# Performance work log

Measured on AMD Instinct MI355X. Metric: run time of the kernel, lower is better.

Reference implementation:

```python
import jax, jax.numpy as jnp
import numpy as np

N_EMBD = 1024
N_HEAD = 16
HEAD_SIZE = N_EMBD // N_HEAD  # 64
BLOCK_SIZE = 2048
HIDDEN = 2 * N_EMBD  # SwiGLU hidden
LN_EPS = 1e-5


def layernorm(x, w, b):
    m = jnp.mean(x, axis=-1, keepdims=True)
    v = jnp.mean(jnp.square(x - m), axis=-1, keepdims=True)
    return (x - m) * jax.lax.rsqrt(v + LN_EPS) * w + b


def rotate_half(x):
    # interleaved halves, exactly as the torch code: stack((-x2, x1)).reshape
    x1 = x[..., 0::2]
    x2 = x[..., 1::2]
    return jnp.stack((-x2, x1), axis=-1).reshape(x.shape)


def rope_tables(T, hd):
    inv_freq = 1.0 / (10000.0 ** (jnp.arange(0, hd, 2, dtype=jnp.float32) / hd))
    t = jnp.arange(T, dtype=jnp.float32)
    freqs = t[:, None] * inv_freq[None, :]           # [T, hd/2]
    emb = jnp.concatenate([freqs, freqs], axis=-1)   # [T, hd]
    return jnp.cos(emb), jnp.sin(emb)


def setup_inputs() -> dict:
    key = jax.random.key(0)
    ks = jax.random.split(key, 12)
    s = 0.02
    d = {
        "x": jax.random.normal(ks[0], (2, BLOCK_SIZE, N_EMBD), dtype=jnp.float32),
        "ln1_w": jnp.ones((N_EMBD,), jnp.float32),
        "ln1_b": jnp.zeros((N_EMBD,), jnp.float32),
        "ln2_w": jnp.ones((N_EMBD,), jnp.float32),
        "ln2_b": jnp.zeros((N_EMBD,), jnp.float32),
        # per-head projections, stored (H, C, hd); equivalent to x @ W.T in torch
        "Wq": jax.random.normal(ks[1], (N_HEAD, N_EMBD, HEAD_SIZE), jnp.float32) * s,
        "Wk": jax.random.normal(ks[2], (N_HEAD, N_EMBD, HEAD_SIZE), jnp.float32) * s,
        "Wv": jax.random.normal(ks[3], (N_HEAD, N_EMBD, HEAD_SIZE), jnp.float32) * s,
        "proj_w": jax.random.normal(ks[4], (N_EMBD, N_EMBD), jnp.float32) * s,
        "proj_b": jnp.zeros((N_EMBD,), jnp.float32),
        # SwiGLU MLP
        "w_w": jax.random.normal(ks[5], (N_EMBD, HIDDEN), jnp.float32) * s,
        "w_b": jnp.zeros((HIDDEN,), jnp.float32),
        "v_w": jax.random.normal(ks[6], (N_EMBD, HIDDEN), jnp.float32) * s,
        "v_b": jnp.zeros((HIDDEN,), jnp.float32),
        "p_w": jax.random.normal(ks[7], (HIDDEN, N_EMBD), jnp.float32) * s,
        "p_b": jnp.zeros((N_EMBD,), jnp.float32),
    }
    return d


def reference(x, ln1_w, ln1_b, ln2_w, ln2_b, Wq, Wk, Wv, proj_w, proj_b,
              w_w, w_b, v_w, v_b, p_w, p_b):
    B, T, C = x.shape
    # --- attention sub-block ---
    h = layernorm(x, ln1_w, ln1_b)
    q = jnp.einsum('btc,hcd->bhtd', h, Wq)
    k = jnp.einsum('btc,hcd->bhtd', h, Wk)
    v = jnp.einsum('btc,hcd->bhtd', h, Wv)
    cos, sin = rope_tables(T, HEAD_SIZE)  # [T, hd]
    cos = cos[None, None]
    sin = sin[None, None]
    q = q * cos + rotate_half(q) * sin
    k = k * cos + rotate_half(k) * sin
    scale = 1.0 / jnp.sqrt(jnp.float32(HEAD_SIZE))
    scores = jnp.einsum('bhtd,bhsd->bhts', q, k) * scale  # [B,H,T,T]
    causal = jnp.tril(jnp.ones((T, T), dtype=bool))
    scores = jnp.where(causal[None, None], scores, -jnp.inf)
    att = jax.nn.softmax(scores, axis=-1)
    o = jnp.einsum('bhts,bhsd->bhtd', att, v)
    o = o.transpose(0, 2, 1, 3).reshape(B, T, C)  # concat heads
    sa = o @ proj_w + proj_b
    x = x + sa
    # --- SwiGLU FFN sub-block ---
    h2 = layernorm(x, ln2_w, ln2_b)
    a = h2 @ w_w + w_b
    a = a * jax.nn.sigmoid(a)  # swish
    b = h2 @ v_w + v_b
    ff = (a * b) @ p_w + p_b
    return x + ff
```

## Files before the change

### kernel.cpp

```cpp
#include <hip/hip_runtime.h>
#include <math.h>

#define N_EMBD    1024
#define N_HEAD    16
#define HEAD_SIZE 64
#define T_SEQ     2048
#define BATCH     2
#define HIDDEN    2048
#define ROWS      4096

typedef __attribute__((ext_vector_type(8))) short bf16x8;
typedef __attribute__((ext_vector_type(4))) float f32x4;
typedef __attribute__((ext_vector_type(16))) float f32x16;
typedef unsigned short u16;

__device__ __forceinline__ u16 f2bf(float x) {
    union { float f; unsigned u; } v; v.f = x;
    unsigned r = v.u + 0x7fffu + ((v.u >> 16) & 1u);
    return (u16)(r >> 16);
}
__device__ __forceinline__ float bf2f(u16 h) {
    union { unsigned u; float f; } v; v.u = ((unsigned)h) << 16;
    return v.f;
}
__device__ __forceinline__ unsigned cvtpk_bf16(float lo, float hi) {
    unsigned r;
    asm volatile("v_cvt_pk_bf16_f32 %0, %1, %2" : "=v"(r) : "v"(lo), "v"(hi));
    return r;
}
__device__ __forceinline__ void gload16(const void* g, void* lds) {
    __builtin_amdgcn_global_load_lds((const __attribute__((address_space(1))) void*)g,
                                     (__attribute__((address_space(3))) void*)lds, 16, 0, 0);
}

__device__ __forceinline__ void wtrans_body(const float* s, u16* d, int ldS, int ldD,
                                            int k0, int n0, float Ts[64][65])
{
    const int tid = threadIdx.x;
    const int rr = tid >> 4, c4 = (tid & 15) * 4;
#pragma unroll
    for (int i = 0; i < 4; i++) {
        float4 v = *(const float4*)(s + (size_t)(k0 + rr + i * 16) * ldS + n0 + c4);
        Ts[rr + i * 16][c4 + 0] = v.x;
        Ts[rr + i * 16][c4 + 1] = v.y;
        Ts[rr + i * 16][c4 + 2] = v.z;
        Ts[rr + i * 16][c4 + 3] = v.w;
    }
    __syncthreads();
    const int nr = tid >> 2, kc = (tid & 3) * 16;
#pragma unroll
    for (int j = 0; j < 4; j++) {
        u16 t0 = f2bf(Ts[kc + j * 4 + 0][nr]);
        u16 t1 = f2bf(Ts[kc + j * 4 + 1][nr]);
        u16 t2 = f2bf(Ts[kc + j * 4 + 2][nr]);
        u16 t3 = f2bf(Ts[kc + j * 4 + 3][nr]);
        *(ushort4*)(d + (size_t)(n0 + nr) * ldD + k0 + kc + j * 4) = make_ushort4(t0, t1, t2, t3);
    }
}

__global__ __launch_bounds__(256) void wtrans_all(const float* __restrict__ Wq, const float* __restrict__ Wk,
                                                  const float* __restrict__ Wv, const float* __restrict__ ww,
                                                  const float* __restrict__ vv, const float* __restrict__ pw,
                                                  const float* __restrict__ ppw,
                                                  u16* __restrict__ Wqkv, u16* __restrict__ wwT,
                                                  u16* __restrict__ vvT, u16* __restrict__ pwT,
                                                  u16* __restrict__ ppT)
{
    __shared__ float Ts[64][65];
    const int b = blockIdx.x;
    const float* s; u16* d; int ldS, ldD, k0, n0;
    if (b < 768) {
        const int z = b >> 4;
        k0 = (b & 15) * 64; n0 = 0;
        const int which = z >> 4;
        s = (which == 0 ? Wq : which == 1 ? Wk : Wv) + (size_t)(z & 15) * 65536;
        d = Wqkv + (size_t)z * 65536;
        ldS = 64; ldD = 1024;
    } else if (b < 1792) {
        const int b2 = b - 768, z = b2 >> 4;
        k0 = (b2 & 15) * 64; n0 = (z & 31) * 64;
        s = (z >> 5) ? vv : ww; d = (z >> 5) ? vvT : wwT;
        ldS = 2048; ldD = 1024;
    } else if (b < 2048) {
        const int b3 = b - 1792;
        k0 = (b3 & 15) * 64; n0 = (b3 >> 4) * 64;
        s = pw; d = pwT; ldS = 1024; ldD = 1024;
    } else {
        const int b4 = b - 2048;
        k0 = (b4 & 31) * 64; n0 = (b4 >> 5) * 64;
        s = ppw; d = ppT; ldS = 1024; ldD = 2048;
    }
    wtrans_body(s, d, ldS, ldD, k0, n0, Ts);
}

__global__ __launch_bounds__(256) void ln_kernel(const float* __restrict__ x,
                                                 const float* __restrict__ w,
                                                 const float* __restrict__ b,
                                                 u16* __restrict__ out)
{
    const int row = blockIdx.x;
    const int tid = threadIdx.x;
    const float* xr = x + (size_t)row * N_EMBD;
    float4 v = *(const float4*)(xr + tid * 4);
    float s  = v.x + v.y + v.z + v.w;
    float s2 = v.x*v.x + v.y*v.y + v.z*v.z + v.w*v.w;
#pragma unroll
    for (int off = 32; off; off >>= 1) {
        s  += __shfl_xor(s, off);
        s2 += __shfl_xor(s2, off);
    }
    __shared__ float ss[4], ss2[4];
    if ((tid & 63) == 0) { ss[tid >> 6] = s; ss2[tid >> 6] = s2; }
    __syncthreads();
    s  = ss[0] + ss[1] + ss[2] + ss[3];
    s2 = ss2[0] + ss2[1] + ss2[2] + ss2[3];
    const float mean = s * (1.0f / N_EMBD);
    const float var  = s2 * (1.0f / N_EMBD) - mean * mean;
    const float rstd = rsqrtf(var + 1e-5f);
    float4 wv = *(const float4*)(w + tid * 4);
    float4 bv = *(const float4*)(b + tid * 4);
    ushort4 st = make_ushort4(f2bf((v.x - mean) * rstd * wv.x + bv.x),
                              f2bf((v.y - mean) * rstd * wv.y + bv.y),
                              f2bf((v.z - mean) * rstd * wv.z + bv.z),
                              f2bf((v.w - mean) * rstd * wv.w + bv.w));
    *(ushort4*)(out + (size_t)row * N_EMBD + tid * 4) = st;
}

__global__ __launch_bounds__(256) void rope_kernel(u16* __restrict__ q, u16* __restrict__ k)
{
    const int u = blockIdx.x * 256 + threadIdx.x;
    const int i  = u & 31;
    const int t  = (u >> 5) & (T_SEQ - 1);
    const int bh = u >> 16;
    const size_t base = ((size_t)bh * T_SEQ + t) * HEAD_SIZE + 2 * i;
    const float L = 0.28782313662425572f;
    const float QS = 0.125f * 1.44269504088896f;
    const int i0 = (2 * i) & 31, i1 = (2 * i + 1) & 31;
    float c0, s0, c1, s1;
    sincosf((float)t * __expf(-(float)i0 * L), &s0, &c0);
    sincosf((float)t * __expf(-(float)i1 * L), &s1, &c1);
    float a0 = bf2f(q[base]), a1 = bf2f(q[base + 1]);
    q[base]     = f2bf((a0 * c0 - a1 * s0) * QS);
    q[base + 1] = f2bf((a1 * c1 + a0 * s1) * QS);
    float b0 = bf2f(k[base]), b1 = bf2f(k[base + 1]);
    k[base]     = f2bf(b0 * c0 - b1 * s0);
    k[base + 1] = f2bf(b1 * c1 + b0 * s1);
}

__global__ __launch_bounds__(256) void gemm_br(const u16* __restrict__ A, const u16* __restrict__ Bt,
                                               const float* __restrict__ bias, const float* __restrict__ resid,
                                               float* __restrict__ Cf,
                                               int N, int K)
{
    __shared__ __align__(16) u16 As[2][128 * 64];
    __shared__ __align__(16) u16 Bs[2][64 * 64];
    const int tid = threadIdx.x, w = tid >> 6, l = tid & 63, l15 = l & 15, l4 = l >> 4;
    const int wm = w >> 1, wn = w & 1;
    const int n0 = blockIdx.x * 64, m0 = blockIdx.y * 128;
    f32x4 acc[4][2] = {};
    const int NT = K >> 6;

    auto stage = [&](int buf, int k0) {
#pragma unroll
        for (int c = 0; c < 4; c++) {
            const int slot = c * 256 + tid;
            const int row = slot >> 3;
            const int sw = ((slot & 7) * 16) ^ ((row & 7) << 4);
            gload16((const char*)(A + (size_t)(m0 + row) * K + k0) + sw, (char*)&As[buf][0] + slot * 16);
        }
#pragma unroll
        for (int c = 0; c < 2; c++) {
            const int slot = c * 256 + tid;
            const int row = slot >> 3;
            const int sw = ((slot & 7) * 16) ^ ((row & 7) << 4);
            gload16((const char*)(Bt + (size_t)(n0 + row) * K + k0) + sw, (char*)&Bs[buf][0] + slot * 16);
        }
    };

    stage(0, 0);
    __syncthreads();
    int cur = 0;
    for (int t = 0; t < NT; t++) {
        if (t + 1 < NT) stage(cur ^ 1, (t + 1) << 6);
#pragma unroll
        for (int ks = 0; ks < 2; ks++) {
            const int cb = ks * 64 + l4 * 16;
            bf16x8 af[4], bf[2];
#pragma unroll
            for (int mt = 0; mt < 4; mt++) {
                const int row = wm * 64 + mt * 16 + l15;
                af[mt] = *(const bf16x8*)((const char*)&As[cur][0] + row * 128 + (cb ^ ((row & 7) << 4)));
            }
#pragma unroll
            for (int u = 0; u < 2; u++) {
                const int row = wn * 32 + u * 16 + l15;
                bf[u] = *(const bf16x8*)((const char*)&Bs[cur][0] + row * 128 + (cb ^ ((row & 7) << 4)));
            }
#pragma unroll
            for (int mt = 0; mt < 4; mt++)
#pragma unroll
                for (int u = 0; u < 2; u++)
                    acc[mt][u] = __builtin_amdgcn_mfma_f32_16x16x32_bf16(af[mt], bf[u], acc[mt][u], 0, 0, 0);
        }
        __syncthreads();
        cur ^= 1;
    }
#pragma unroll
    for (int mt = 0; mt < 4; mt++) {
#pragma unroll
        for (int u = 0; u < 2; u++) {
            const int n = n0 + wn * 32 + u * 16 + l15;
            const float bi = bias[n];
#pragma unroll
            for (int r = 0; r < 4; r++) {
                const int m = m0 + wm * 64 + mt * 16 + l4 * 4 + r;
                const size_t idx = (size_t)m * N + n;
                Cf[idx] = acc[mt][u][r] + bi + resid[idx];
            }
        }
    }
}

__global__ __launch_bounds__(256, 4) void gemm_qkv(const u16* __restrict__ A, const u16* __restrict__ Bt,
                                                   u16* __restrict__ qo, u16* __restrict__ ko, u16* __restrict__ vto)
{
    __shared__ __align__(16) u16 As[2][64 * 64];
    __shared__ __align__(16) u16 Bs[2][64 * 64];
    const int tid = threadIdx.x, w = tid >> 6, l = tid & 63, l15 = l & 15, l4 = l >> 4;
    const int wm = w >> 1, wn = w & 1;
    const int n0 = blockIdx.x * 128, m0 = blockIdx.y * 128;
    const int K = N_EMBD;
    f32x4 acc[4][4] = {};
    const int NT = K >> 5;

    auto stage = [&](int buf, int k0) {
#pragma unroll
        for (int c = 0; c < 2; c++) {
            const int slot = c * 256 + tid;
            const int r2 = slot >> 3;
            const int w16u = (slot & 7) ^ (r2 & 7);
            const int grow = (w16u >> 2) * 64 + r2;
            const int kc = w16u & 3;
            gload16(A  + (size_t)(m0 + grow) * K + k0 + kc * 8, (char*)&As[buf][0] + slot * 16);
            gload16(Bt + (size_t)(n0 + grow) * K + k0 + kc * 8, (char*)&Bs[buf][0] + slot * 16);
        }
    };

    stage(0, 0);
    __syncthreads();
    int cur = 0;
    for (int t = 0; t < NT; t++) {
        if (t + 1 < NT) stage(cur ^ 1, (t + 1) << 5);
        bf16x8 af[4], bf[4];
#pragma unroll
        for (int q4 = 0; q4 < 4; q4++) {
            const int ga = wm * 64 + q4 * 16 + l15;
            const int ra = ga & 63, ha = ga >> 6;
            af[q4] = *(const bf16x8*)((const char*)&As[cur][0] + ra * 128 + (((ha << 2) | l4) ^ (ra & 7)) * 16);
            const int gb = wn * 64 + q4 * 16 + l15;
            const int rb = gb & 63, hb = gb >> 6;
            bf[q4] = *(const bf16x8*)((const char*)&Bs[cur][0] + rb * 128 + (((hb << 2) | l4) ^ (rb & 7)) * 16);
        }
#pragma unroll
        for (int mt = 0; mt < 4; mt++)
#pragma unroll
            for (int nt = 0; nt < 4; nt++)
                acc[mt][nt] = __builtin_amdgcn_mfma_f32_16x16x32_bf16(af[mt], bf[nt], acc[mt][nt], 0, 0, 0);
        __syncthreads();
        cur ^= 1;
    }
#pragma unroll
    for (int mt = 0; mt < 4; mt++) {
#pragma unroll
        for (int nt = 0; nt < 4; nt++) {
            const int n = n0 + wn * 64 + nt * 16 + l15;
            const int which = n >> 10, hd = (n >> 6) & 15, dd = n & 63;
            const int mb = m0 + wm * 64 + mt * 16 + l4 * 4;
            const int bI = mb >> 11, tq = mb & (T_SEQ - 1);
            if (which == 2) {
                ushort4 st = make_ushort4(f2bf(acc[mt][nt][0]), f2bf(acc[mt][nt][1]),
                                          f2bf(acc[mt][nt][2]), f2bf(acc[mt][nt][3]));
                *(ushort4*)(vto + ((size_t)(bI * N_HEAD + hd) * HEAD_SIZE + dd) * T_SEQ + tq) = st;
            } else {
                u16* dst = (which == 0) ? qo : ko;
#pragma unroll
                for (int r = 0; r < 4; r++)
                    dst[((size_t)(bI * N_HEAD + hd) * T_SEQ + tq + r) * HEAD_SIZE + dd] = f2bf(acc[mt][nt][r]);
            }
        }
    }
}

__global__ __launch_bounds__(256, 4) void gemm_glu(const u16* __restrict__ A, const u16* __restrict__ Bw,
                                                   const u16* __restrict__ Bv,
                                                   const float* __restrict__ wb, const float* __restrict__ vb,
                                                   u16* __restrict__ G)
{
    __shared__ __align__(16) u16 As[2][64 * 64];
    __shared__ __align__(16) u16 Bws[2][32 * 64];
    __shared__ __align__(16) u16 Bvs[2][32 * 64];
    const int tid = threadIdx.x, w = tid >> 6, l = tid & 63, l15 = l & 15, l4 = l >> 4;
    const int wm = w >> 1, wn = w & 1;
    const int n0 = blockIdx.x * 64, m0 = blockIdx.y * 128;
    const int K = N_EMBD;
    f32x4 accA[4][2] = {};
    f32x4 accB[4][2] = {};
    const int NT = K >> 5;

    auto stage = [&](int buf, int k0) {
#pragma unroll
        for (int c = 0; c < 2; c++) {
            const int slot = c * 256 + tid;
            const int r2 = slot >> 3;
            const int w16u = (slot & 7) ^ (r2 & 7);
            const int grow = (w16u >> 2) * 64 + r2;
            const int kc = w16u & 3;
            gload16(A + (size_t)(m0 + grow) * K + k0 + kc * 8, (char*)&As[buf][0] + slot * 16);
        }
        {
            const int slot = tid;
            const int r2 = slot >> 3;
            const int w16u = (slot & 7) ^ (r2 & 7);
            const int grow = (w16u >> 2) * 32 + r2;
            const int kc = w16u & 3;
            gload16(Bw + (size_t)(n0 + grow) * K + k0 + kc * 8, (char*)&Bws[buf][0] + slot * 16);
            gload16(Bv + (size_t)(n0 + grow) * K + k0 + kc * 8, (char*)&Bvs[buf][0] + slot * 16);
        }
    };

    stage(0, 0);
    __syncthreads();
    int cur = 0;
    for (int t = 0; t < NT; t++) {
        if (t + 1 < NT) stage(cur ^ 1, (t + 1) << 5);
        bf16x8 af[4], bwf[2], bvf[2];
#pragma unroll
        for (int q4 = 0; q4 < 4; q4++) {
            const int ga = wm * 64 + q4 * 16 + l15;
            const int ra = ga & 63, ha = ga >> 6;
            af[q4] = *(const bf16x8*)((const char*)&As[cur][0] + ra * 128 + (((ha << 2) | l4) ^ (ra & 7)) * 16);
        }
#pragma unroll
        for (int u = 0; u < 2; u++) {
            const int gb = wn * 32 + u * 16 + l15;
            const int rb = gb & 31, hb = gb >> 5;
            const int off = rb * 128 + (((hb << 2) | l4) ^ (rb & 7)) * 16;
            bwf[u] = *(const bf16x8*)((const char*)&Bws[cur][0] + off);
            bvf[u] = *(const bf16x8*)((const char*)&Bvs[cur][0] + off);
        }
#pragma unroll
        for (int mt = 0; mt < 4; mt++)
#pragma unroll
            for (int u = 0; u < 2; u++) {
                accA[mt][u] = __builtin_amdgcn_mfma_f32_16x16x32_bf16(af[mt], bwf[u], accA[mt][u], 0, 0, 0);
                accB[mt][u] = __builtin_amdgcn_mfma_f32_16x16x32_bf16(af[mt], bvf[u], accB[mt][u], 0, 0, 0);
            }
        __syncthreads();
        cur ^= 1;
    }
#pragma unroll
    for (int mt = 0; mt < 4; mt++) {
#pragma unroll
        for (int u = 0; u < 2; u++) {
            const int n = n0 + wn * 32 + u * 16 + l15;
            const float wbi = wb[n], vbi = vb[n];
#pragma unroll
            for (int r = 0; r < 4; r++) {
                const int m = m0 + wm * 64 + mt * 16 + l4 * 4 + r;
                const float a  = accA[mt][u][r] + wbi;
                const float bb = accB[mt][u][r] + vbi;
                G[(size_t)m * HIDDEN + n] = f2bf(a / (1.f + __expf(-a)) * bb);
            }
        }
    }
}

__global__ __launch_bounds__(256, 4) void attn_mfma(const u16* __restrict__ q, const u16* __restrict__ k,
                                                    const u16* __restrict__ vt, u16* __restrict__ o)
{
    __shared__ __align__(16) u16 Kb[2][64 * 64];
    __shared__ __align__(16) u16 Vb[2][64 * 64];
    __shared__ float ml[2][32];
    const int tid = threadIdx.x, l = tid & 63, l31 = l & 31, hh2 = (l >> 5) & 1;
    const int wid  = tid >> 6;
    const int qsub = wid >> 1;
    const int par  = wid & 1;
    const int bh  = blockIdx.x;
    const int y = blockIdx.y;
    const int qtb = ((y & 8) == 0) ? y : ((y < 16) ? 23 - y : (y < 24 ? y : 55 - y));
    const int qt  = qtb * 2 + qsub;
    const int qw0 = qt * 32;
    const int nc  = qtb + 1;
    const u16* qb  = q  + (size_t)bh * T_SEQ * HEAD_SIZE;
    const u16* kbg = k  + (size_t)bh * T_SEQ * HEAD_SIZE;
    const u16* vbg = vt + (size_t)bh * HEAD_SIZE * T_SEQ;

    bf16x8 qf[4];
    {
        const u16* qr = qb + (size_t)(qw0 + l31) * HEAD_SIZE + hh2 * 8;
#pragma unroll
        for (int kk = 0; kk < 4; kk++) qf[kk] = *(const bf16x8*)(qr + kk * 16);
    }
    bf16x8 onesf;
#pragma unroll
    for (int e = 0; e < 8; e++) onesf[e] = (short)0x3F80;

    f32x16 oacc0 = {}, oacc1 = {}, lacc = {};
    const float M0 = 20.f;

    auto stage = [&](int buf, int s0) {
#pragma unroll
        for (int c = 0; c < 2; c++) {
            const int slot = c * 256 + tid;
            const int row = slot >> 3;
            const int sw = ((slot & 7) * 16) ^ ((row & 7) << 4);
            gload16((const char*)(kbg + (size_t)(s0 + row) * HEAD_SIZE) + sw, (char*)&Kb[buf][0] + slot * 16);
        }
#pragma unroll
        for (int c = 0; c < 2; c++) {
            const int slot = c * 256 + tid;
            const int row = slot >> 3;
            const int sw = ((slot & 7) * 16) ^ ((row & 7) << 4);
            gload16((const char*)(vbg + (size_t)row * T_SEQ + s0) + sw, (char*)&Vb[buf][0] + slot * 16);
        }
    };

    stage(0, 0);
    __syncthreads();
    int cur = 0;

    for (int j = 0; j < nc; j++) {
        if (j + 1 < nc) stage(cur ^ 1, (j + 1) * 64);

        const int hc = 2 * j + par;
        if (hc <= qt) {
            f32x16 sa;
#pragma unroll
            for (int reg = 0; reg < 16; reg++) sa[reg] = -M0;
            const int row = par * 32 + l31;
            const int swz = (row & 7) << 4;
#pragma unroll
            for (int kk = 0; kk < 4; kk++) {
                const bf16x8 kf = *(const bf16x8*)((const char*)&Kb[cur][0] + row * 128 + ((kk * 32 + hh2 * 16) ^ swz));
                sa = __builtin_amdgcn_mfma_f32_32x32x16_bf16(kf, qf[kk], sa, 0, 0, 0);
            }
            if (hc == qt) {
#pragma unroll
                for (int reg = 0; reg < 16; reg++) {
                    const int R = (reg & 3) + 8 * (reg >> 2) + 4 * hh2;
                    if (R > l31) sa[reg] = -1e30f;
                }
            }
#pragma unroll
            for (int reg = 0; reg < 16; reg++) sa[reg] = exp2f(sa[reg]);

            unsigned pk[8];
#pragma unroll
            for (int jj = 0; jj < 8; jj++) pk[jj] = cvtpk_bf16(sa[2 * jj], sa[2 * jj + 1]);

#pragma unroll
            for (int st = 0; st < 2; st++) {
                const int b = st * 4;
                union { unsigned u[4]; bf16x8 v; } r;
                const unsigned s0w = (unsigned)__shfl_xor((int)pk[b + 0], 32);
                const unsigned s1w = (unsigned)__shfl_xor((int)pk[b + 1], 32);
                const unsigned s2w = (unsigned)__shfl_xor((int)pk[b + 2], 32);
                const unsigned s3w = (unsigned)__shfl_xor((int)pk[b + 3], 32);
                r.u[0] = hh2 ? s2w : pk[b + 0];
                r.u[1] = hh2 ? s3w : pk[b + 1];
                r.u[2] = hh2 ? pk[b + 2] : s0w;
                r.u[3] = hh2 ? pk[b + 3] : s1w;
                lacc = __builtin_amdgcn_mfma_f32_32x32x16_bf16(onesf, r.v, lacc, 0, 0, 0);
#pragma unroll
                for (int dt = 0; dt < 2; dt++) {
                    const int vrow = dt * 32 + l31;
                    const int vswz = (vrow & 7) << 4;
                    const int vcol = (par * 64 + st * 32 + hh2 * 16) ^ vswz;
                    const bf16x8 vf = *(const bf16x8*)((const char*)&Vb[cur][0] + vrow * 128 + vcol);
                    if (dt == 0) oacc0 = __builtin_amdgcn_mfma_f32_32x32x16_bf16(vf, r.v, oacc0, 0, 0, 0);
                    else         oacc1 = __builtin_amdgcn_mfma_f32_32x32x16_bf16(vf, r.v, oacc1, 0, 0, 0);
                }
            }
        }
        __syncthreads();
        cur ^= 1;
    }

    float* obuf = (float*)&Kb[0][0] + (size_t)qsub * 2048;
    if (par == 1) {
#pragma unroll
        for (int reg = 0; reg < 16; reg++) {
            const int R = (reg & 3) + 8 * (reg >> 2) + 4 * hh2;
            obuf[R * 32 + l31] = oacc0[reg];
            obuf[(32 + R) * 32 + l31] = oacc1[reg];
        }
        if (hh2 == 0) ml[qsub][l31] = lacc[0];
    }
    __syncthreads();
    if (par == 0) {
        const float inv = 1.f / (lacc[0] + ml[qsub][l31]);
        const int bI = bh >> 4, hd = bh & 15;
        u16* ob = o + ((size_t)(bI * T_SEQ + qw0 + l31)) * N_EMBD + hd * HEAD_SIZE;
#pragma unroll
        for (int g = 0; g < 4; g++) {
            const int d0a = g * 8 + hh2 * 4;
            float v0[4], v1[4];
#pragma unroll
            for (int r = 0; r < 4; r++) {
                const int R = d0a + r;
                v0[r] = (oacc0[4 * g + r] + obuf[R * 32 + l31]) * inv;
                v1[r] = (oacc1[4 * g + r] + obuf[(32 + R) * 32 + l31]) * inv;
            }
            *(ushort4*)(ob + d0a)      = make_ushort4(f2bf(v0[0]), f2bf(v0[1]), f2bf(v0[2]), f2bf(v0[3]));
            *(ushort4*)(ob + 32 + d0a) = make_ushort4(f2bf(v1[0]), f2bf(v1[1]), f2bf(v1[2]), f2bf(v1[3]));
        }
    }
}

extern "C" void kernel_launch(void* const* d_in, const int* in_sizes, int n_in,
                              void* d_out, int out_size, void* d_ws, size_t ws_size,
                              hipStream_t stream)
{
    (void)in_sizes; (void)n_in; (void)out_size; (void)ws_size;
    const float* x      = (const float*)d_in[0];
    const float* ln1_w  = (const float*)d_in[1];
    const float* ln1_b  = (const float*)d_in[2];
    const float* ln2_w  = (const float*)d_in[3];
    const float* ln2_b  = (const float*)d_in[4];
    const float* Wq     = (const float*)d_in[5];
    const float* Wk     = (const float*)d_in[6];
    const float* Wv     = (const float*)d_in[7];
    const float* proj_w = (const float*)d_in[8];
    const float* proj_b = (const float*)d_in[9];
    const float* w_w    = (const float*)d_in[10];
    const float* w_b    = (const float*)d_in[11];
    const float* v_w    = (const float*)d_in[12];
    const float* v_b    = (const float*)d_in[13];
    const float* p_w    = (const float*)d_in[14];
    const float* p_b    = (const float*)d_in[15];
    float* out = (float*)d_out;

    char* W = (char*)d_ws;
    u16*   Wqkv = (u16*)(W + 0);
    u16*   pwT  = (u16*)(W + 6291456);
    u16*   wwT  = (u16*)(W + 8388608);
    u16*   vvT  = (u16*)(W + 12582912);
    u16*   ppT  = (u16*)(W + 16777216);
    u16*   h    = (u16*)(W + 20971520);
    u16*   qB   = (u16*)(W + 29360128);
    u16*   kB   = (u16*)(W + 37748736);
    u16*   vtB  = (u16*)(W + 46137344);
    u16*   oB   = (u16*)(W + 54525952);
    float* x1   = (float*)(W + 62914560);
    u16*   ga   = qB;

    wtrans_all<<<2560, 256, 0, stream>>>(Wq, Wk, Wv, w_w, v_w, proj_w, p_w,
                                         Wqkv, wwT, vvT, pwT, ppT);

    ln_kernel<<<ROWS, 256, 0, stream>>>(x, ln1_w, ln1_b, h);
    gemm_qkv<<<dim3(24, 32), 256, 0, stream>>>(h, Wqkv, qB, kB, vtB);
    rope_kernel<<<(BATCH * N_HEAD * T_SEQ * 32) / 256, 256, 0, stream>>>(qB, kB);
    attn_mfma<<<dim3(BATCH * N_HEAD, T_SEQ / 64), 256, 0, stream>>>(qB, kB, vtB, oB);
    gemm_br<<<dim3(16, 32), 256, 0, stream>>>(oB, pwT, proj_b, x, x1, N_EMBD, N_EMBD);
    ln_kernel<<<ROWS, 256, 0, stream>>>(x1, ln2_w, ln2_b, h);
    gemm_glu<<<dim3(32, 32), 256, 0, stream>>>(h, wwT, vvT, w_b, v_b, ga);
    gemm_br<<<dim3(16, 32), 256, 0, stream>>>(ga, ppT, p_b, x1, out, N_EMBD, HIDDEN);
}
```

Before: 204.4 us.

## Shrink residual GEMM tiles to 64x64 and simplify attention block ordering

The bias+residual GEMM moves from 128x64 tiles with a 64-wide K step to 64x64 tiles with a 32-wide K step. Each staging load now covers both operands with a new swizzled LDS layout, launch bounds request 4 blocks per CU, and the grid doubles to 1024 blocks. This aims to fill the MI355X CUs better for the 4096x1024 outputs, at the cost of less data reuse per tile and twice as many K iterations and barriers. Attention blocks are also remapped to run the longest causal query tiles first, replacing the previous interleaved ordering.

```diff
diff --git a/kernel.cpp b/kernel.cpp
--- a/kernel.cpp
+++ b/kernel.cpp
@@ -147,73 +147,64 @@
     k[base + 1] = f2bf(b1 * c1 + b0 * s1);
 }
 
-__global__ __launch_bounds__(256) void gemm_br(const u16* __restrict__ A, const u16* __restrict__ Bt,
-                                               const float* __restrict__ bias, const float* __restrict__ resid,
-                                               float* __restrict__ Cf,
-                                               int N, int K)
-{
-    __shared__ __align__(16) u16 As[2][128 * 64];
-    __shared__ __align__(16) u16 Bs[2][64 * 64];
+__global__ __launch_bounds__(256, 4) void gemm_br(const u16* __restrict__ A, const u16* __restrict__ Bt,
+                                                  const float* __restrict__ bias, const float* __restrict__ resid,
+                                                  float* __restrict__ Cf,
+                                                  int N, int K)
+{
+    __shared__ __align__(16) u16 As[2][32 * 64];
+    __shared__ __align__(16) u16 Bs[2][32 * 64];
     const int tid = threadIdx.x, w = tid >> 6, l = tid & 63, l15 = l & 15, l4 = l >> 4;
     const int wm = w >> 1, wn = w & 1;
-    const int n0 = blockIdx.x * 64, m0 = blockIdx.y * 128;
-    f32x4 acc[4][2] = {};
-    const int NT = K >> 6;
+    const int n0 = blockIdx.x * 64, m0 = blockIdx.y * 64;
+    f32x4 acc[2][2] = {};
+    const int NT = K >> 5;
 
     auto stage = [&](int buf, int k0) {
-#pragma unroll
-        for (int c = 0; c < 4; c++) {
-            const int slot = c * 256 + tid;
-            const int row = slot >> 3;
-            const int sw = ((slot & 7) * 16) ^ ((row & 7) << 4);
-            gload16((const char*)(A + (size_t)(m0 + row) * K + k0) + sw, (char*)&As[buf][0] + slot * 16);
-        }
-#pragma unroll
-        for (int c = 0; c < 2; c++) {
-            const int slot = c * 256 + tid;
-            const int row = slot >> 3;
-            const int sw = ((slot & 7) * 16) ^ ((row & 7) << 4);
-            gload16((const char*)(Bt + (size_t)(n0 + row) * K + k0) + sw, (char*)&Bs[buf][0] + slot * 16);
-        }
+        const int slot = tid;
+        const int r2 = slot >> 3;
+        const int w16u = (slot & 7) ^ (r2 & 7);
+        const int grow = (w16u >> 2) * 32 + r2;
+        const int kc = w16u & 3;
+        gload16(A  + (size_t)(m0 + grow) * K + k0 + kc * 8, (char*)&As[buf][0] + slot * 16);
+        gload16(Bt + (size_t)(n0 + grow) * K + k0 + kc * 8, (char*)&Bs[buf][0] + slot * 16);
     };
 
     stage(0, 0);
     __syncthreads();
     int cur = 0;
     for (int t = 0; t < NT; t++) {
-        if (t + 1 < NT) stage(cur ^ 1, (t + 1) << 6);
-#pragma unroll
-        for (int ks = 0; ks < 2; ks++) {
-            const int cb = ks * 64 + l4 * 16;
-            bf16x8 af[4], bf[2];
-#pragma unroll
-            for (int mt = 0; mt < 4; mt++) {
-                const int row = wm * 64 + mt * 16 + l15;
-                af[mt] = *(const bf16x8*)((const char*)&As[cur][0] + row * 128 + (cb ^ ((row & 7) << 4)));
-            }
-#pragma unroll
-            for (int u = 0; u < 2; u++) {
-                const int row = wn * 32 + u * 16 + l15;
-                bf[u] = *(const bf16x8*)((const char*)&Bs[cur][0] + row * 128 + (cb ^ ((row & 7) << 4)));
-            }
-#pragma unroll
-            for (int mt = 0; mt < 4; mt++)
-#pragma unroll
-                for (int u = 0; u < 2; u++)
-                    acc[mt][u] = __builtin_amdgcn_mfma_f32_16x16x32_bf16(af[mt], bf[u], acc[mt][u], 0, 0, 0);
-        }
+        if (t + 1 < NT) stage(cur ^ 1, (t + 1) << 5);
+        bf16x8 af[2], bf[2];
+#pragma unroll
+        for (int mt = 0; mt < 2; mt++) {
+            const int ga = wm * 32 + mt * 16 + l15;
+            const int ra = ga & 31, ha = ga >> 5;
+            af[mt] = *(const bf16x8*)((const char*)&As[cur][0] + ra * 128 + (((ha << 2) | l4) ^ (ra & 7)) * 16);
+        }
+#pragma unroll
+        for (int u = 0; u < 2; u++) {
+            const int gb = wn * 32 + u * 16 + l15;
+            const int rb = gb & 31, hb = gb >> 5;
+            bf[u] = *(const bf16x8*)((const char*)&Bs[cur][0] + rb * 128 + (((hb << 2) | l4) ^ (rb & 7)) * 16);
+        }
+#pragma unroll
+        for (int mt = 0; mt < 2; mt++)
+#pragma unroll
+            for (int u = 0; u < 2; u++)
+                acc[mt][u] = __builtin_amdgcn_mfma_f32_16x16x32_bf16(af[mt], bf[u], acc[mt][u], 0, 0, 0);
         __syncthreads();
         cur ^= 1;
     }
 #pragma unroll
-    for (int mt = 0; mt < 4; mt++) {
+    for (int mt = 0; mt < 2; mt++) {
 #pragma unroll
         for (int u = 0; u < 2; u++) {
             const int n = n0 + wn * 32 + u * 16 + l15;
             const float bi = bias[n];
 #pragma unroll
             for (int r = 0; r < 4; r++) {
-                const int m = m0 + wm * 64 + mt * 16 + l4 * 4 + r;
+                const int m = m0 + wm * 32 + mt * 16 + l4 * 4 + r;
                 const size_t idx = (size_t)m * N + n;
                 Cf[idx] = acc[mt][u][r] + bi + resid[idx];
             }
@@ -386,8 +377,7 @@
     const int qsub = wid >> 1;
     const int par  = wid & 1;
     const int bh  = blockIdx.x;
-    const int y = blockIdx.y;
-    const int qtb = ((y & 8) == 0) ? y : ((y < 16) ? 23 - y : (y < 24 ? y : 55 - y));
+    const int qtb = (int)gridDim.y - 1 - (int)blockIdx.y;
     const int qt  = qtb * 2 + qsub;
     const int qw0 = qt * 32;
     const int nc  = qtb + 1;
@@ -561,8 +551,8 @@
     gemm_qkv<<<dim3(24, 32), 256, 0, stream>>>(h, Wqkv, qB, kB, vtB);
     rope_kernel<<<(BATCH * N_HEAD * T_SEQ * 32) / 256, 256, 0, stream>>>(qB, kB);
     attn_mfma<<<dim3(BATCH * N_HEAD, T_SEQ / 64), 256, 0, stream>>>(qB, kB, vtB, oB);
-    gemm_br<<<dim3(16, 32), 256, 0, stream>>>(oB, pwT, proj_b, x, x1, N_EMBD, N_EMBD);
+    gemm_br<<<dim3(16, 64), 256, 0, stream>>>(oB, pwT, proj_b, x, x1, N_EMBD, N_EMBD);
     ln_kernel<<<ROWS, 256, 0, stream>>>(x1, ln2_w, ln2_b, h);
     gemm_glu<<<dim3(32, 32), 256, 0, stream>>>(h, wwT, vvT, w_b, v_b, ga);
-    gemm_br<<<dim3(16, 32), 256, 0, stream>>>(ga, ppT, p_b, x1, out, N_EMBD, HIDDEN);
-}
+    gemm_br<<<dim3(16, 64), 256, 0, stream>>>(ga, ppT, p_b, x1, out, N_EMBD, HIDDEN);
+}
```

Measured after the change: 205.8 us. No clear change (+0.7%).
